# Performance work log

Hardware: AMD Instinct MI355X
Metric: run time of the kernel (lower is better)

The kernel has to match this reference:

```python
import jax, jax.numpy as jnp
import numpy as np

N = 50000      # nodes
E = 800000     # edges (before self loops)
F_IN = 512     # input feature dim (num_features)
D = 128        # hidden_dim
NBLK = 3       # num_layers - 1
EPS = 1e-5


def _layernorm(x, g, b):
    mu = x.mean(-1, keepdims=True)
    var = ((x - mu) ** 2).mean(-1, keepdims=True)
    return (x - mu) / jnp.sqrt(var + EPS) * g + b


def _gatv2(x, Wl, bl, Wr, br, att, bias, src, dst, n):
    # PyG GATv2Conv, heads=1, eval mode (attention dropout off), self loops in src/dst
    xl = x @ Wl + bl                      # [N, D] messages (x_j side)
    xr = x @ Wr + br                      # [N, D] target side (x_i)
    e = jax.nn.leaky_relu(xl[src] + xr[dst], negative_slope=0.2)  # [E', D]
    score = e @ att                       # [E']
    smax = jax.ops.segment_max(score, dst, num_segments=n)
    ex = jnp.exp(score - smax[dst])
    denom = jax.ops.segment_sum(ex, dst, num_segments=n)
    alpha = ex / denom[dst]               # segment softmax over incoming edges
    out = jax.ops.segment_sum(alpha[:, None] * xl[src], dst, num_segments=n)
    return out + bias


def setup_inputs() -> dict:
    key = jax.random.key(0)
    ks = jax.random.split(key, 32)
    w = lambda k, shape: (jax.random.normal(k, shape, jnp.float32) * 0.02)
    p = {}
    p["x"] = jax.random.normal(ks[0], (N, F_IN), jnp.float32)
    p["edge_index"] = jax.random.randint(ks[1], (2, E), 0, N)
    p["emb_W"] = w(ks[2], (F_IN, D)); p["emb_b"] = jnp.zeros((D,), jnp.float32)
    p["ln1_g"] = jnp.ones((NBLK, D), jnp.float32); p["ln1_b"] = jnp.zeros((NBLK, D), jnp.float32)
    p["gat_Wl"] = w(ks[3], (NBLK, D, D)); p["gat_bl"] = jnp.zeros((NBLK, D), jnp.float32)
    p["gat_Wr"] = w(ks[4], (NBLK, D, D)); p["gat_br"] = jnp.zeros((NBLK, D), jnp.float32)
    p["gat_att"] = w(ks[5], (NBLK, D)); p["gat_bias"] = jnp.zeros((NBLK, D), jnp.float32)
    for i in range(NBLK):
        h = D * (i + 1)  # mlp_ratio = level = i+1
        p[f"mlp_w1_{i}"] = w(ks[6 + 2 * i], (D, h))
        p[f"mlp_w2_{i}"] = w(ks[7 + 2 * i], (h, D))
    p["attn_Wa"] = w(ks[12], (D, D)); p["attn_ba"] = jnp.zeros((D,), jnp.float32)
    p["attn_Wb"] = w(ks[13], (D, D)); p["attn_bb"] = jnp.zeros((D,), jnp.float32)
    p["attn_Wc"] = w(ks[14], (D, 1)); p["attn_bc"] = jnp.zeros((1,), jnp.float32)
    p["rho_W"] = w(ks[15], (D, D)); p["rho_b"] = jnp.zeros((D,), jnp.float32)
    p["cls_W"] = w(ks[16], (D, 4)); p["cls_b"] = jnp.zeros((4,), jnp.float32)
    return p


def reference(x, edge_index, emb_W, emb_b, ln1_g, ln1_b, gat_Wl, gat_bl, gat_Wr, gat_br,
              gat_att, gat_bias, mlp_w1_0, mlp_w2_0, mlp_w1_1, mlp_w2_1, mlp_w1_2, mlp_w2_2,
              attn_Wa, attn_ba, attn_Wb, attn_bb, attn_Wc, attn_bc, rho_W, rho_b, cls_W, cls_b):
    n = x.shape[0]
    sl = jnp.arange(n, dtype=edge_index.dtype)
    src = jnp.concatenate([edge_index[0], sl])  # add self loops (GATv2Conv default)
    dst = jnp.concatenate([edge_index[1], sl])
    h = jax.nn.relu(x @ emb_W + emb_b)          # embedding (dropout off)
    mlps = [(mlp_w1_0, mlp_w2_0), (mlp_w1_1, mlp_w2_1), (mlp_w1_2, mlp_w2_2)]
    for i in range(NBLK):
        hn = _layernorm(h, ln1_g[i], ln1_b[i])
        h = h + _gatv2(hn, gat_Wl[i], gat_bl[i], gat_Wr[i], gat_br[i], gat_att[i], gat_bias[i], src, dst, n)
        w1, w2 = mlps[i]
        # NOTE: original forward applies channel_mix directly on x (norm2 is unused)
        h = h + jax.nn.gelu(h @ w1, approximate=False) @ w2
    # Attn_Net_Gated pooling
    a = jnp.tanh(h @ attn_Wa + attn_ba)
    b = jax.nn.sigmoid(h @ attn_Wb + attn_bb)
    A = ((a * b) @ attn_Wc + attn_bc).T          # [1, N]
    h_path = jax.nn.softmax(A, axis=1) @ h       # [1, D]
    hr = jax.nn.relu(h_path @ rho_W + rho_b)
    logits = hr @ cls_W + cls_b                  # [1, 4]
    Y_hat = jnp.argmax(logits, axis=1, keepdims=True)
    hazards = jax.nn.sigmoid(logits)
    S = jnp.cumprod(1.0 - hazards, axis=1)
    return (hazards, S, Y_hat, logits)
```

## Files before the change

### kernel.cpp

```cpp
#include <hip/hip_runtime.h>
#include <math.h>


#define D 128
#define NBLK 3

typedef __attribute__((ext_vector_type(8))) short bf16x8;
typedef __attribute__((ext_vector_type(4))) float f32x4;

static __device__ __forceinline__ float wred_sum(float v) {
#pragma unroll
    for (int m = 1; m < 64; m <<= 1) v += __shfl_xor(v, m, 64);
    return v;
}

static __device__ __forceinline__ float bf2f(unsigned short u) {
    union { unsigned i; float f; } c; c.i = ((unsigned)u) << 16; return c.f;
}
static __device__ __forceinline__ unsigned short f2bf(float f) {
    union { float f; unsigned i; } c; c.f = f;
    unsigned r = c.i + 0x7fff + ((c.i >> 16) & 1);
    return (unsigned short)(r >> 16);
}

static __device__ __forceinline__ void gl16(const unsigned short* g, unsigned short* l) {
    __builtin_amdgcn_global_load_lds((const __attribute__((address_space(1))) void*)g,
                                     (__attribute__((address_space(3))) void*)l, 16, 0, 0);
}

__global__ void zero_k(int* deg, int* fill, float* red, int n) {
    int i = blockIdx.x * blockDim.x + threadIdx.x;
    if (i < n) { deg[i] = 0; fill[i] = 0; }
    if (i < 132) red[i] = 0.f;
}

__global__ void hist_k(const int* __restrict__ dst, int* __restrict__ deg, int E) {
    int e = blockIdx.x * blockDim.x + threadIdx.x;
    if (e < E) atomicAdd(&deg[dst[e]], 1);
}

__global__ __launch_bounds__(256) void blockscan_k(const int* __restrict__ deg,
                                                   int* __restrict__ rowptr,
                                                   int* __restrict__ bsum, int n) {
    __shared__ int tmp[256];
    const int tid = threadIdx.x;
    const int i = blockIdx.x * 256 + tid;
    int v = (i < n) ? deg[i] : 0;
    tmp[tid] = v;
    __syncthreads();
#pragma unroll
    for (int off = 1; off < 256; off <<= 1) {
        int t = (tid >= off) ? tmp[tid - off] : 0;
        __syncthreads();
        tmp[tid] += t;
        __syncthreads();
    }
    if (i < n) rowptr[i + 1] = tmp[tid];
    if (tid == 255) bsum[blockIdx.x] = tmp[255];
}

__global__ __launch_bounds__(256) void scansums_k(int* __restrict__ bsum, int nb) {
    __shared__ int tmp[256];
    const int tid = threadIdx.x;
    int v = (tid < nb) ? bsum[tid] : 0;
    tmp[tid] = v;
    __syncthreads();
#pragma unroll
    for (int off = 1; off < 256; off <<= 1) {
        int t = (tid >= off) ? tmp[tid - off] : 0;
        __syncthreads();
        tmp[tid] += t;
        __syncthreads();
    }
    if (tid < nb) bsum[tid] = tmp[tid];
}

__global__ __launch_bounds__(256) void addoff_k(int* __restrict__ rowptr,
                                                const int* __restrict__ bsum, int n) {
    int i = blockIdx.x * 256 + threadIdx.x;
    if (i == 0) rowptr[0] = 0;
    if (i < n && blockIdx.x > 0) rowptr[i + 1] += bsum[blockIdx.x - 1];
}

__global__ void scatter_k(const int* __restrict__ src, const int* __restrict__ dst,
                          const int* __restrict__ rowptr, int* __restrict__ fill,
                          int* __restrict__ esrc, int E) {
    int e = blockIdx.x * blockDim.x + threadIdx.x;
    if (e < E) {
        int d = dst[e];
        int pos = rowptr[d] + atomicAdd(&fill[d], 1);
        esrc[pos] = src[e];
    }
}

struct WDesc { const float* s; unsigned short* d; int K; int M; };
struct WPack { WDesc w[21]; };

__global__ __launch_bounds__(256) void wprep_k(WPack p) {
    WDesc d = p.w[blockIdx.y];
    const int nc = d.K / 32;
    const int chunks = (d.M / 16) * nc * 64;
    for (int i = blockIdx.x * 256 + threadIdx.x; i < chunks; i += gridDim.x * 256) {
        const int l = i & 63;
        const int c = (i >> 6) % nc;
        const int t = i / (64 * nc);
        const int m = t * 16 + (l & 15);
        const int kb = c * 32 + ((l >> 4) & 3) * 8;
#pragma unroll
        for (int j = 0; j < 8; ++j)
            d.d[(size_t)i * 8 + j] = f2bf(d.s[(size_t)(kb + j) * d.M + m]);
    }
}

__global__ __launch_bounds__(256) void bcat_k(const float* bl, const float* br,
                                              const float* ba, const float* bb,
                                              float* sb) {
    const int t = threadIdx.x;
    for (int i = 0; i < 3; ++i)
        sb[i * 256 + t] = (t < 128) ? bl[i * 128 + t] : br[i * 128 + t - 128];
    sb[3 * 256 + t] = (t < 128) ? ba[t] : bb[t - 128];
}

template <int NR, bool KM, int ACT, bool BIAS, bool ACC, bool LNM, bool A16,
          bool W32, bool W16>
__global__ __launch_bounds__(256) void rgemm_k(const void* __restrict__ Ap,
                                               const unsigned short* __restrict__ BTc,
                                               const float* __restrict__ bias,
                                               const float* __restrict__ lng,
                                               const float* __restrict__ lnb,
                                               float* __restrict__ C32,
                                               unsigned short* __restrict__ C16,
                                               int N, int strideA, int M) {
    __shared__ unsigned short Bls[128 * 128];
    const int tid = threadIdx.x;
    const int w = tid >> 6, l = tid & 63;
    const int q = l >> 4;
    int r = blockIdx.x * 64 + w * 16 + (l & 15);
    if (r > N - 1) r = N - 1;

    bf16x8 afr[4];
    auto loadA = [&](int koff) {
        if (A16) {
            const unsigned short* A = (const unsigned short*)Ap;
#pragma unroll
            for (int c = 0; c < 4; ++c)
                afr[c] = *(const bf16x8*)(A + (size_t)r * strideA + koff + c * 32 + q * 8);
        } else {
            const float* A = (const float*)Ap;
            float av[4][8];
#pragma unroll
            for (int c = 0; c < 4; ++c) {
                const float* ap = A + (size_t)r * strideA + koff + c * 32 + q * 8;
                const float4 v0 = *(const float4*)ap;
                const float4 v1 = *(const float4*)(ap + 4);
                av[c][0] = v0.x; av[c][1] = v0.y; av[c][2] = v0.z; av[c][3] = v0.w;
                av[c][4] = v1.x; av[c][5] = v1.y; av[c][6] = v1.z; av[c][7] = v1.w;
            }
            if (LNM) {
                float s = 0.f;
#pragma unroll
                for (int c = 0; c < 4; ++c)
#pragma unroll
                    for (int j = 0; j < 8; ++j) s += av[c][j];
                s += __shfl_xor(s, 16, 64); s += __shfl_xor(s, 32, 64);
                const float mu = s * (1.f / 128.f);
                float vv = 0.f;
#pragma unroll
                for (int c = 0; c < 4; ++c)
#pragma unroll
                    for (int j = 0; j < 8; ++j) { const float dd = av[c][j] - mu; vv += dd * dd; }
                vv += __shfl_xor(vv, 16, 64); vv += __shfl_xor(vv, 32, 64);
                const float rs = rsqrtf(vv * (1.f / 128.f) + 1e-5f);
#pragma unroll
                for (int c = 0; c < 4; ++c) {
                    const int kb = c * 32 + q * 8;
                    const float4 g0 = *(const float4*)(lng + kb);
                    const float4 g1 = *(const float4*)(lng + kb + 4);
                    const float4 b0 = *(const float4*)(lnb + kb);
                    const float4 b1 = *(const float4*)(lnb + kb + 4);
                    const float gg[8] = {g0.x, g0.y, g0.z, g0.w, g1.x, g1.y, g1.z, g1.w};
                    const float bb[8] = {b0.x, b0.y, b0.z, b0.w, b1.x, b1.y, b1.z, b1.w};
#pragma unroll
                    for (int j = 0; j < 8; ++j)
                        av[c][j] = (av[c][j] - mu) * rs * gg[j] + bb[j];
                }
            }
#pragma unroll
            for (int c = 0; c < 4; ++c)
#pragma unroll
                for (int j = 0; j < 8; ++j) afr[c][j] = (short)f2bf(av[c][j]);
        }
    };

    f32x4 acc[8];
#pragma unroll
    for (int t = 0; t < 8; ++t) acc[t] = (f32x4){0.f, 0.f, 0.f, 0.f};

    if (!KM) loadA(0);

    const int rb = blockIdx.x * 64 + w * 16 + q * 4;
    auto epi = [&](int col0) {
#pragma unroll
        for (int t = 0; t < 8; ++t) {
            const int col = col0 + t * 16 + (l & 15);
            const float bv = BIAS ? bias[col] : 0.f;
#pragma unroll
            for (int rr = 0; rr < 4; ++rr) {
                const int row = rb + rr;
                if (row >= N) continue;
                float xv = acc[t][rr] + bv;
                if (ACC) xv += C32[(size_t)row * M + col];
                if (ACT == 1) xv = fmaxf(xv, 0.f);
                else if (ACT == 2) xv = 0.5f * xv * (1.f + erff(xv * 0.70710678118654752f));
                else if (ACT == 5) xv = (col < 128) ? tanhf(xv) : 1.f / (1.f + expf(-xv));
                if (W32) C32[(size_t)row * M + col] = xv;
                if (W16) C16[(size_t)row * M + col] = f2bf(xv);
            }
        }
    };

#pragma unroll
    for (int rnd = 0; rnd < NR; ++rnd) {
        if (rnd) __syncthreads();
        const unsigned short* bsrc = BTc + (size_t)rnd * 16384;
#pragma unroll
        for (int i = 0; i < 8; ++i) {
            const int idx = i * 256 + tid;
            gl16(bsrc + (size_t)idx * 8, &Bls[idx * 8]);
        }
        if (KM) loadA(rnd * 128);
        __syncthreads();
#pragma unroll
        for (int c = 0; c < 4; ++c)
#pragma unroll
            for (int t = 0; t < 8; ++t) {
                const bf16x8 bfr = *(const bf16x8*)&Bls[((t * 4 + c) * 64 + l) * 8];
                acc[t] = __builtin_amdgcn_mfma_f32_16x16x32_bf16(afr[c], bfr, acc[t], 0, 0, 0);
            }
        if (!KM) {
            epi(rnd * 128);
#pragma unroll
            for (int t = 0; t < 8; ++t) acc[t] = (f32x4){0.f, 0.f, 0.f, 0.f};
        }
    }
    if (KM) epi(0);
}

__global__ __launch_bounds__(256) void gat3_k(const unsigned short* __restrict__ X,
                                              const float* __restrict__ att,
                                              const float* __restrict__ gbias,
                                              const int* __restrict__ rowptr,
                                              const int* __restrict__ esrc,
                                              float* __restrict__ H, int n) {
    const int l = threadIdx.x & 63;
    const int node = blockIdx.x * 4 + (threadIdx.x >> 6);
    if (node >= n) return;
    const int q = l >> 4;
    const int d0 = (l & 15) * 8;

    float a8[8], xr[8], xs[8];
    {
        const float4 t0 = *(const float4*)&att[d0];
        const float4 t1 = *(const float4*)&att[d0 + 4];
        a8[0] = t0.x; a8[1] = t0.y; a8[2] = t0.z; a8[3] = t0.w;
        a8[4] = t1.x; a8[5] = t1.y; a8[6] = t1.z; a8[7] = t1.w;
        const bf16x8 uxs = *(const bf16x8*)&X[(size_t)node * 256 + d0];
        const bf16x8 uxr = *(const bf16x8*)&X[(size_t)node * 256 + 128 + d0];
#pragma unroll
        for (int j = 0; j < 8; ++j) {
            xs[j] = bf2f((unsigned short)uxs[j]);
            xr[j] = bf2f((unsigned short)uxr[j]);
        }
    }

    float sc = 0.f;
#pragma unroll
    for (int j = 0; j < 8; ++j) {
        const float e = xs[j] + xr[j];
        sc = fmaf(a8[j], fmaxf(e, 0.2f * e), sc);
    }
#pragma unroll
    for (int m = 1; m < 16; m <<= 1) sc += __shfl_xor(sc, m, 64);
    const float wself = __expf(sc);
    float dsum = (q == 0) ? wself : 0.f;
    float acc[8];
#pragma unroll
    for (int j = 0; j < 8; ++j) acc[j] = (q == 0) ? wself * xs[j] : 0.f;

    const int p1 = rowptr[node + 1];
    int p = rowptr[node] + q;
    bool v0 = p < p1, v1 = p + 4 < p1, v2 = p + 8 < p1;
    int i2 = v2 ? esrc[p + 8] : 0;
    bf16x8 u0, u1;
    if (v0) u0 = *(const bf16x8*)&X[(size_t)esrc[p] * 256 + d0];
    if (v1) u1 = *(const bf16x8*)&X[(size_t)esrc[p + 4] * 256 + d0];
    while (v0) {
        bf16x8 u2;
        if (v2) u2 = *(const bf16x8*)&X[(size_t)i2 * 256 + d0];
        const bool v3 = p + 12 < p1;
        const int i3 = v3 ? esrc[p + 12] : 0;

        float xl[8];
#pragma unroll
        for (int j = 0; j < 8; ++j) xl[j] = bf2f((unsigned short)u0[j]);
        float e_sc = 0.f;
#pragma unroll
        for (int j = 0; j < 8; ++j) {
            const float e = xl[j] + xr[j];
            e_sc = fmaf(a8[j], fmaxf(e, 0.2f * e), e_sc);
        }
#pragma unroll
        for (int m = 1; m < 16; m <<= 1) e_sc += __shfl_xor(e_sc, m, 64);
        const float wgt = __expf(e_sc);
        dsum += wgt;
#pragma unroll
        for (int j = 0; j < 8; ++j) acc[j] = fmaf(wgt, xl[j], acc[j]);

        u0 = u1; u1 = u2; i2 = i3;
        v0 = v1; v1 = v2; v2 = v3;
        p += 4;
    }

#pragma unroll
    for (int m = 16; m < 64; m <<= 1) {
        dsum += __shfl_xor(dsum, m, 64);
#pragma unroll
        for (int j = 0; j < 8; ++j) acc[j] += __shfl_xor(acc[j], m, 64);
    }

    if (q == 0) {
        const float inv = 1.f / dsum;
        const size_t o = (size_t)node * D + d0;
        float4 h0 = *(const float4*)&H[o];
        float4 h1 = *(const float4*)&H[o + 4];
        float hv[8] = {h0.x, h0.y, h0.z, h0.w, h1.x, h1.y, h1.z, h1.w};
#pragma unroll
        for (int j = 0; j < 8; ++j) hv[j] += acc[j] * inv + gbias[d0 + j];
        *(float4*)&H[o]     = make_float4(hv[0], hv[1], hv[2], hv[3]);
        *(float4*)&H[o + 4] = make_float4(hv[4], hv[5], hv[6], hv[7]);
    }
}

__global__ __launch_bounds__(256) void poolws_k(const float* __restrict__ P,
                                                const float* __restrict__ Wc,
                                                const float* __restrict__ bc,
                                                const float* __restrict__ H,
                                                float* __restrict__ red, int n) {
    const int lane = threadIdx.x & 63;
    const int gw = blockIdx.x * 4 + (threadIdx.x >> 6);
    const int nw = gridDim.x * 4;
    const float wc0 = Wc[lane], wc1 = Wc[64 + lane];
    const float bcv = bc[0];
    float a0 = 0.f, a1 = 0.f, dn = 0.f;
    for (int node = gw; node < n; node += nw) {
        const size_t o = (size_t)node * 256;
        const float v = wred_sum(P[o + lane] * P[o + 128 + lane] * wc0 +
                                 P[o + 64 + lane] * P[o + 192 + lane] * wc1);
        const float wgt = __expf(v + bcv);
        dn += wgt;
        a0 = fmaf(wgt, H[(size_t)node * D + lane], a0);
        a1 = fmaf(wgt, H[(size_t)node * D + 64 + lane], a1);
    }
    atomicAdd(&red[lane], a0);
    atomicAdd(&red[64 + lane], a1);
    if (lane == 0) atomicAdd(&red[128], dn);
}

__global__ __launch_bounds__(128) void final_k(const float* __restrict__ red,
                                               const float* __restrict__ rho_W,
                                               const float* __restrict__ rho_b,
                                               const float* __restrict__ cls_W,
                                               const float* __restrict__ cls_b,
                                               float* __restrict__ out) {
    __shared__ float hp[128];
    __shared__ float hr[128];
    __shared__ float lg[4];
    const int t = threadIdx.x;
    hp[t] = red[t] / red[128];
    __syncthreads();
    float s = rho_b[t];
    for (int k = 0; k < 128; ++k) s = fmaf(hp[k], rho_W[k * 128 + t], s);
    hr[t] = fmaxf(s, 0.f);
    __syncthreads();
    if (t < 4) {
        float l = cls_b[t];
        for (int k = 0; k < 128; ++k) l = fmaf(hr[k], cls_W[k * 4 + t], l);
        lg[t] = l;
    }
    __syncthreads();
    if (t == 0) {
        float hz[4], S[4];
        for (int c = 0; c < 4; ++c) hz[c] = 1.f / (1.f + expf(-lg[c]));
        S[0] = 1.f - hz[0];
        for (int c = 1; c < 4; ++c) S[c] = S[c - 1] * (1.f - hz[c]);
        int am = 0; float bm = lg[0];
        for (int c = 1; c < 4; ++c) if (lg[c] > bm) { bm = lg[c]; am = c; }
        out[0] = hz[0]; out[1] = hz[1]; out[2] = hz[2]; out[3] = hz[3];
        out[4] = S[0];  out[5] = S[1];  out[6] = S[2];  out[7] = S[3];
        out[8] = (float)am;
        out[9] = lg[0]; out[10] = lg[1]; out[11] = lg[2]; out[12] = lg[3];
    }
}

static inline int cdiv(int a, int b) { return (a + b - 1) / b; }

extern "C" void kernel_launch(void* const* d_in, const int* in_sizes, int n_in,
                              void* d_out, int out_size, void* d_ws, size_t ws_size,
                              hipStream_t stream) {
    const float* x      = (const float*)d_in[0];
    const int*   ei     = (const int*)d_in[1];
    const float* emb_W  = (const float*)d_in[2];
    const float* emb_b  = (const float*)d_in[3];
    const float* ln1_g  = (const float*)d_in[4];
    const float* ln1_b  = (const float*)d_in[5];
    const float* gat_Wl = (const float*)d_in[6];
    const float* gat_bl = (const float*)d_in[7];
    const float* gat_Wr = (const float*)d_in[8];
    const float* gat_br = (const float*)d_in[9];
    const float* gat_att  = (const float*)d_in[10];
    const float* gat_bias = (const float*)d_in[11];
    const float* mlp_w1[NBLK] = {(const float*)d_in[12], (const float*)d_in[14], (const float*)d_in[16]};
    const float* mlp_w2[NBLK] = {(const float*)d_in[13], (const float*)d_in[15], (const float*)d_in[17]};
    const float* attn_Wa = (const float*)d_in[18];
    const float* attn_ba = (const float*)d_in[19];
    const float* attn_Wb = (const float*)d_in[20];
    const float* attn_bb = (const float*)d_in[21];
    const float* attn_Wc = (const float*)d_in[22];
    const float* attn_bc = (const float*)d_in[23];
    const float* rho_W   = (const float*)d_in[24];
    const float* rho_b   = (const float*)d_in[25];
    const float* cls_W   = (const float*)d_in[26];
    const float* cls_b   = (const float*)d_in[27];
    float* out = (float*)d_out;

    const int N = in_sizes[0] / 512;
    const int E = in_sizes[1] / 2;
    const int* src = ei;
    const int* dst = ei + E;

    char* base = (char*)d_ws;
    float* P = (float*)base;
    float* H = P + (size_t)N * 256;
    unsigned short* X = (unsigned short*)(H + (size_t)N * D);
    unsigned short* T = X + (size_t)N * 256;
    float* red  = (float*)(T + (size_t)N * 384);
    float* sb   = red + 132;
    unsigned short* wbuf = (unsigned short*)(sb + 1024);
    int* esrc   = (int*)(wbuf + 393216);
    int* deg    = esrc + E;
    int* rowptr = deg + N;
    int* fill   = rowptr + N + 1;
    int* bsum   = fill + N;

    unsigned short* embT = wbuf;
    unsigned short* gatT = wbuf + 4 * 16384;
    unsigned short* w1T0 = gatT + 6 * 16384;
    unsigned short* w1T1 = w1T0 + 16384;
    unsigned short* w1T2 = w1T1 + 2 * 16384;
    unsigned short* w2T0 = w1T2 + 3 * 16384;
    unsigned short* w2T1 = w2T0 + 16384;
    unsigned short* w2T2 = w2T1 + 2 * 16384;
    unsigned short* attT = w2T2 + 3 * 16384;
    unsigned short* w1T[NBLK] = {w1T0, w1T1, w1T2};
    unsigned short* w2T[NBLK] = {w2T0, w2T1, w2T2};

    const int nb = cdiv(N, 256);
    zero_k<<<cdiv(N, 256), 256, 0, stream>>>(deg, fill, red, N);
    hist_k<<<cdiv(E, 256), 256, 0, stream>>>(dst, deg, E);
    blockscan_k<<<nb, 256, 0, stream>>>(deg, rowptr, bsum, N);
    scansums_k<<<1, 256, 0, stream>>>(bsum, nb);
    addoff_k<<<nb, 256, 0, stream>>>(rowptr, bsum, N);
    scatter_k<<<cdiv(E, 256), 256, 0, stream>>>(src, dst, rowptr, fill, esrc, E);

    {
        WPack p;
        int di = 0;
        for (int r = 0; r < 4; ++r)
            p.w[di++] = {emb_W + (size_t)r * 128 * 128, embT + (size_t)r * 16384, 128, 128};
        for (int i = 0; i < 3; ++i) {
            p.w[di++] = {gat_Wl + (size_t)i * 16384, gatT + (size_t)(2 * i) * 16384, 128, 128};
            p.w[di++] = {gat_Wr + (size_t)i * 16384, gatT + (size_t)(2 * i + 1) * 16384, 128, 128};
        }
        for (int i = 0; i < 3; ++i)
            p.w[di++] = {mlp_w1[i], w1T[i], 128, 128 * (i + 1)};
        for (int i = 0; i < 3; ++i)
            for (int r = 0; r <= i; ++r)
                p.w[di++] = {mlp_w2[i] + (size_t)r * 128 * 128, w2T[i] + (size_t)r * 16384, 128, 128};
        p.w[di++] = {attn_Wa, attT, 128, 128};
        p.w[di++] = {attn_Wb, attT + 16384, 128, 128};
        wprep_k<<<dim3(32, 21), 256, 0, stream>>>(p);
    }
    bcat_k<<<1, 256, 0, stream>>>(gat_bl, gat_br, attn_ba, attn_bb, sb);

    const int gx = cdiv(N, 64);

    rgemm_k<4, true, 1, true, false, false, false, true, false>
        <<<gx, 256, 0, stream>>>(x, embT, emb_b, nullptr, nullptr,
                                 H, nullptr, N, 512, 128);

    for (int i = 0; i < NBLK; ++i) {
        rgemm_k<2, false, 0, true, false, true, false, false, true>
            <<<gx, 256, 0, stream>>>(H, gatT + (size_t)(2 * i) * 16384, sb + i * 256,
                                     ln1_g + i * D, ln1_b + i * D, nullptr, X, N, 128, 256);
        gat3_k<<<cdiv(N, 4), 256, 0, stream>>>(X, gat_att + i * D, gat_bias + i * D,
                                               rowptr, esrc, H, N);
        const int h = D * (i + 1);
        if (i == 0)
            rgemm_k<1, false, 2, false, false, false, false, false, true>
                <<<gx, 256, 0, stream>>>(H, w1T[i], nullptr, nullptr, nullptr,
                                         nullptr, T, N, 128, h);
        else if (i == 1)
            rgemm_k<2, false, 2, false, false, false, false, false, true>
                <<<gx, 256, 0, stream>>>(H, w1T[i], nullptr, nullptr, nullptr,
                                         nullptr, T, N, 128, h);
        else
            rgemm_k<3, false, 2, false, false, false, false, false, true>
                <<<gx, 256, 0, stream>>>(H, w1T[i], nullptr, nullptr, nullptr,
                                         nullptr, T, N, 128, h);
        if (i == 0)
            rgemm_k<1, true, 0, false, true, false, true, true, false>
                <<<gx, 256, 0, stream>>>(T, w2T[i], nullptr, nullptr, nullptr,
                                         H, nullptr, N, h, 128);
        else if (i == 1)
            rgemm_k<2, true, 0, false, true, false, true, true, false>
                <<<gx, 256, 0, stream>>>(T, w2T[i], nullptr, nullptr, nullptr,
                                         H, nullptr, N, h, 128);
        else
            rgemm_k<3, true, 0, false, true, false, true, true, false>
                <<<gx, 256, 0, stream>>>(T, w2T[i], nullptr, nullptr, nullptr,
                                         H, nullptr, N, h, 128);
    }

    rgemm_k<2, false, 5, true, false, false, false, true, false>
        <<<gx, 256, 0, stream>>>(H, attT, sb + 3 * 256, nullptr, nullptr,
                                 P, nullptr, N, 128, 256);
    poolws_k<<<120, 256, 0, stream>>>(P, attn_Wc, attn_bc, H, red, N);
    final_k<<<1, 128, 0, stream>>>(red, rho_W, rho_b, cls_W, cls_b, out);
}
```

Baseline: 748.2 us.

## Fuse gated attention GEMM with pooling and use per-block partial sums

Replaces the separate attention-projection GEMM (which wrote a 256-wide fp32 P buffer), the pooling kernel and its global atomics with one kernel. That kernel computes tanh/sigmoid gates from MFMA results in registers, forms per-row attention weights, and accumulates weighted H within the block. Per-block partial sums are written to slots and reduced in the final kernel. This removes the round trip of P through memory and the second read of H. The cost is a serial single-block reduction over all slots in the final kernel.

Measured after the change: 876.3 us. +17.1%, slower.

```diff
diff --git a/kernel.cpp b/kernel.cpp
--- a/kernel.cpp
+++ b/kernel.cpp
@@ -7,12 +7,6 @@
 
 typedef __attribute__((ext_vector_type(8))) short bf16x8;
 typedef __attribute__((ext_vector_type(4))) float f32x4;
-
-static __device__ __forceinline__ float wred_sum(float v) {
-#pragma unroll
-    for (int m = 1; m < 64; m <<= 1) v += __shfl_xor(v, m, 64);
-    return v;
-}
 
 static __device__ __forceinline__ float bf2f(unsigned short u) {
     union { unsigned i; float f; } c; c.i = ((unsigned)u) << 16; return c.f;
@@ -28,10 +22,9 @@
                                      (__attribute__((address_space(3))) void*)l, 16, 0, 0);
 }
 
-__global__ void zero_k(int* deg, int* fill, float* red, int n) {
+__global__ void zero_k(int* deg, int* fill, int n) {
     int i = blockIdx.x * blockDim.x + threadIdx.x;
     if (i < n) { deg[i] = 0; fill[i] = 0; }
-    if (i < 132) red[i] = 0.f;
 }
 
 __global__ void hist_k(const int* __restrict__ dst, int* __restrict__ deg, int E) {
@@ -212,7 +205,6 @@
                 if (ACC) xv += C32[(size_t)row * M + col];
                 if (ACT == 1) xv = fmaxf(xv, 0.f);
                 else if (ACT == 2) xv = 0.5f * xv * (1.f + erff(xv * 0.70710678118654752f));
-                else if (ACT == 5) xv = (col < 128) ? tanhf(xv) : 1.f / (1.f + expf(-xv));
                 if (W32) C32[(size_t)row * M + col] = xv;
                 if (W16) C16[(size_t)row * M + col] = f2bf(xv);
             }
@@ -341,42 +333,147 @@
     }
 }
 
-__global__ __launch_bounds__(256) void poolws_k(const float* __restrict__ P,
-                                                const float* __restrict__ Wc,
-                                                const float* __restrict__ bc,
-                                                const float* __restrict__ H,
-                                                float* __restrict__ red, int n) {
-    const int lane = threadIdx.x & 63;
-    const int gw = blockIdx.x * 4 + (threadIdx.x >> 6);
-    const int nw = gridDim.x * 4;
-    const float wc0 = Wc[lane], wc1 = Wc[64 + lane];
+__global__ __launch_bounds__(256) void attnpool_k(const float* __restrict__ H,
+                                                  const unsigned short* __restrict__ BTc,
+                                                  const float* __restrict__ bias,
+                                                  const float* __restrict__ Wc,
+                                                  const float* __restrict__ bc,
+                                                  float* __restrict__ slot, int N) {
+    __shared__ unsigned short Bls[128 * 128];
+    __shared__ float sacc[4][128];
+    __shared__ float sdn[4];
+    const int tid = threadIdx.x;
+    const int w = tid >> 6, l = tid & 63;
+    const int q = l >> 4, l15 = l & 15;
+    const int rowbase = blockIdx.x * 64 + w * 16;
+    int r = rowbase + l15;
+    if (r > N - 1) r = N - 1;
+
+    float av[4][8];
+    bf16x8 afr[4];
+#pragma unroll
+    for (int c = 0; c < 4; ++c) {
+        const float* ap = H + (size_t)r * D + c * 32 + q * 8;
+        const float4 v0 = *(const float4*)ap;
+        const float4 v1 = *(const float4*)(ap + 4);
+        av[c][0] = v0.x; av[c][1] = v0.y; av[c][2] = v0.z; av[c][3] = v0.w;
+        av[c][4] = v1.x; av[c][5] = v1.y; av[c][6] = v1.z; av[c][7] = v1.w;
+#pragma unroll
+        for (int j = 0; j < 8; ++j) afr[c][j] = (short)f2bf(av[c][j]);
+    }
+
+    float th[8][4];
+    f32x4 acc[8];
+
+#pragma unroll
+    for (int rnd = 0; rnd < 2; ++rnd) {
+        if (rnd) __syncthreads();
+        const unsigned short* bsrc = BTc + (size_t)rnd * 16384;
+#pragma unroll
+        for (int i = 0; i < 8; ++i) {
+            const int idx = i * 256 + tid;
+            gl16(bsrc + (size_t)idx * 8, &Bls[idx * 8]);
+        }
+#pragma unroll
+        for (int t = 0; t < 8; ++t) acc[t] = (f32x4){0.f, 0.f, 0.f, 0.f};
+        __syncthreads();
+#pragma unroll
+        for (int c = 0; c < 4; ++c)
+#pragma unroll
+            for (int t = 0; t < 8; ++t) {
+                const bf16x8 bfr = *(const bf16x8*)&Bls[((t * 4 + c) * 64 + l) * 8];
+                acc[t] = __builtin_amdgcn_mfma_f32_16x16x32_bf16(afr[c], bfr, acc[t], 0, 0, 0);
+            }
+        if (rnd == 0) {
+#pragma unroll
+            for (int t = 0; t < 8; ++t) {
+                const float bv = bias[t * 16 + l15];
+#pragma unroll
+                for (int rr = 0; rr < 4; ++rr) th[t][rr] = tanhf(acc[t][rr] + bv);
+            }
+        }
+    }
+
+    float pa[4] = {0.f, 0.f, 0.f, 0.f};
+#pragma unroll
+    for (int t = 0; t < 8; ++t) {
+        const float bv = bias[128 + t * 16 + l15];
+        const float wcv = Wc[t * 16 + l15];
+#pragma unroll
+        for (int rr = 0; rr < 4; ++rr) {
+            const float sg = 1.f / (1.f + __expf(-(acc[t][rr] + bv)));
+            pa[rr] = fmaf(th[t][rr] * sg, wcv, pa[rr]);
+        }
+    }
+#pragma unroll
+    for (int m = 1; m < 16; m <<= 1)
+#pragma unroll
+        for (int rr = 0; rr < 4; ++rr) pa[rr] += __shfl_xor(pa[rr], m, 64);
+
     const float bcv = bc[0];
-    float a0 = 0.f, a1 = 0.f, dn = 0.f;
-    for (int node = gw; node < n; node += nw) {
-        const size_t o = (size_t)node * 256;
-        const float v = wred_sum(P[o + lane] * P[o + 128 + lane] * wc0 +
-                                 P[o + 64 + lane] * P[o + 192 + lane] * wc1);
-        const float wgt = __expf(v + bcv);
-        dn += wgt;
-        a0 = fmaf(wgt, H[(size_t)node * D + lane], a0);
-        a1 = fmaf(wgt, H[(size_t)node * D + 64 + lane], a1);
-    }
-    atomicAdd(&red[lane], a0);
-    atomicAdd(&red[64 + lane], a1);
-    if (lane == 0) atomicAdd(&red[128], dn);
-}
-
-__global__ __launch_bounds__(128) void final_k(const float* __restrict__ red,
-                                               const float* __restrict__ rho_W,
-                                               const float* __restrict__ rho_b,
-                                               const float* __restrict__ cls_W,
-                                               const float* __restrict__ cls_b,
-                                               float* __restrict__ out) {
+    float wgt[4];
+#pragma unroll
+    for (int rr = 0; rr < 4; ++rr) {
+        const int row = blockIdx.x * 64 + w * 16 + q * 4 + rr;
+        wgt[rr] = (row < N) ? __expf(pa[rr] + bcv) : 0.f;
+    }
+    float s = wgt[0] + wgt[1] + wgt[2] + wgt[3];
+    s += __shfl_xor(s, 16, 64);
+    s += __shfl_xor(s, 32, 64);
+    if (l == 0) sdn[w] = s;
+
+    const int srcl = (w << 6) ? 0 : 0;
+    const int sl = ((l15 >> 2) << 4);
+    float wv[4];
+#pragma unroll
+    for (int rr = 0; rr < 4; ++rr) wv[rr] = __shfl(wgt[rr], sl, 64);
+    const int rsel = l15 & 3;
+    float wm = (rsel == 0) ? wv[0] : (rsel == 1) ? wv[1] : (rsel == 2) ? wv[2] : wv[3];
+
+#pragma unroll
+    for (int c = 0; c < 4; ++c) {
+        float pv[8];
+#pragma unroll
+        for (int j = 0; j < 8; ++j) pv[j] = wm * av[c][j];
+#pragma unroll
+        for (int m = 1; m < 16; m <<= 1)
+#pragma unroll
+            for (int j = 0; j < 8; ++j) pv[j] += __shfl_xor(pv[j], m, 64);
+        if (l15 == 0) {
+#pragma unroll
+            for (int j = 0; j < 8; ++j) sacc[w][c * 32 + q * 8 + j] = pv[j];
+        }
+    }
+    __syncthreads();
+    if (tid < 128) {
+        const float tot = sacc[0][tid] + sacc[1][tid] + sacc[2][tid] + sacc[3][tid];
+        slot[(size_t)blockIdx.x * 132 + tid] = tot;
+    }
+    if (tid == 0)
+        slot[(size_t)blockIdx.x * 132 + 128] = sdn[0] + sdn[1] + sdn[2] + sdn[3];
+}
+
+__global__ __launch_bounds__(128) void final2_k(const float* __restrict__ slot, int nb,
+                                                const float* __restrict__ rho_W,
+                                                const float* __restrict__ rho_b,
+                                                const float* __restrict__ cls_W,
+                                                const float* __restrict__ cls_b,
+                                                float* __restrict__ out) {
     __shared__ float hp[128];
+    __shared__ float sdn[128];
     __shared__ float hr[128];
     __shared__ float lg[4];
     const int t = threadIdx.x;
-    hp[t] = red[t] / red[128];
+    float a = 0.f, d = 0.f;
+    for (int b = 0; b < nb; ++b) a += slot[(size_t)b * 132 + t];
+    for (int b = t; b < nb; b += 128) d += slot[(size_t)b * 132 + 128];
+    sdn[t] = d;
+    __syncthreads();
+    for (int s = 64; s > 0; s >>= 1) {
+        if (t < s) sdn[t] += sdn[t + s];
+        __syncthreads();
+    }
+    hp[t] = a / sdn[0];
     __syncthreads();
     float s = rho_b[t];
     for (int k = 0; k < 128; ++k) s = fmaf(hp[k], rho_W[k * 128 + t], s);
@@ -437,14 +534,14 @@
     const int E = in_sizes[1] / 2;
     const int* src = ei;
     const int* dst = ei + E;
+    const int gx = cdiv(N, 64);
 
     char* base = (char*)d_ws;
-    float* P = (float*)base;
-    float* H = P + (size_t)N * 256;
+    float* H = (float*)base;
     unsigned short* X = (unsigned short*)(H + (size_t)N * D);
     unsigned short* T = X + (size_t)N * 256;
-    float* red  = (float*)(T + (size_t)N * 384);
-    float* sb   = red + 132;
+    float* slot = (float*)(T + (size_t)N * 384);
+    float* sb   = slot + (size_t)gx * 132;
     unsigned short* wbuf = (unsigned short*)(sb + 1024);
     int* esrc   = (int*)(wbuf + 393216);
     int* deg    = esrc + E;
@@ -465,7 +562,7 @@
     unsigned short* w2T[NBLK] = {w2T0, w2T1, w2T2};
 
     const int nb = cdiv(N, 256);
-    zero_k<<<cdiv(N, 256), 256, 0, stream>>>(deg, fill, red, N);
+    zero_k<<<cdiv(N, 256), 256, 0, stream>>>(deg, fill, N);
     hist_k<<<cdiv(E, 256), 256, 0, stream>>>(dst, deg, E);
     blockscan_k<<<nb, 256, 0, stream>>>(deg, rowptr, bsum, N);
     scansums_k<<<1, 256, 0, stream>>>(bsum, nb);
@@ -491,8 +588,6 @@
         wprep_k<<<dim3(32, 21), 256, 0, stream>>>(p);
     }
     bcat_k<<<1, 256, 0, stream>>>(gat_bl, gat_br, attn_ba, attn_bb, sb);
-
-    const int gx = cdiv(N, 64);
 
     rgemm_k<4, true, 1, true, false, false, false, true, false>
         <<<gx, 256, 0, stream>>>(x, embT, emb_b, nullptr, nullptr,
@@ -531,9 +626,6 @@
                                          H, nullptr, N, h, 128);
     }
 
-    rgemm_k<2, false, 5, true, false, false, false, true, false>
-        <<<gx, 256, 0, stream>>>(H, attT, sb + 3 * 256, nullptr, nullptr,
-                                 P, nullptr, N, 128, 256);
-    poolws_k<<<120, 256, 0, stream>>>(P, attn_Wc, attn_bc, H, red, N);
-    final_k<<<1, 128, 0, stream>>>(red, rho_W, rho_b, cls_W, cls_b, out);
-}
+    attnpool_k<<<gx, 256, 0, stream>>>(H, attT, sb + 3 * 256, attn_Wc, attn_bc, slot, N);
+    final2_k<<<1, 128, 0, stream>>>(slot, gx, rho_W, rho_b, cls_W, cls_b, out);
+}
```
